# Optimization experiments

Measured on AMD Instinct MI355X. Metric: run time of the kernel, lower is better.

The kernel has to match this reference:

```python
import jax, jax.numpy as jnp
import numpy as np

T, B, D = 256, 64, 512


def setup_inputs() -> dict:
    key = jax.random.key(0)
    ks = jax.random.split(key, 9)
    s = 1.0 / np.sqrt(D)  # torch Linear default init scale (uniform), use scaled normal
    return {
        "x": jax.random.normal(ks[0], (T, B, D), dtype=jnp.float32),
        "y": jax.random.normal(ks[1], (T, B, D), dtype=jnp.float32),
        "Wr": jax.random.normal(ks[2], (D, D), dtype=jnp.float32) * s,
        "Ur": jax.random.normal(ks[3], (D, D), dtype=jnp.float32) * s,
        "Wz": jax.random.normal(ks[4], (D, D), dtype=jnp.float32) * s,
        "Uz": jax.random.normal(ks[5], (D, D), dtype=jnp.float32) * s,
        "Wg": jax.random.normal(ks[6], (D, D), dtype=jnp.float32) * s,
        "Ug": jax.random.normal(ks[7], (D, D), dtype=jnp.float32) * s,
        "bg": jnp.full((D,), 2.0, dtype=jnp.float32),
    }


def reference(x, y, Wr, Ur, Wz, Uz, Wg, Ug, bg):
    # GTrXL gating unit. torch Linear(y) == y @ W.T
    r = jax.nn.sigmoid(jnp.einsum("tbd,ed->tbe", y, Wr) + jnp.einsum("tbd,ed->tbe", x, Ur))
    z = jax.nn.sigmoid(jnp.einsum("tbd,ed->tbe", y, Wz) + jnp.einsum("tbd,ed->tbe", x, Uz) - bg)
    h = jnp.tanh(jnp.einsum("tbd,ed->tbe", y, Wg) + jnp.einsum("tbd,ed->tbe", r * x, Ug))
    g = (1.0 - z) * x + z * h  # (T, B, D)
    return g
```

## Files before the change

### kernel.cpp

```cpp
#include <hip/hip_runtime.h>
#include <stdint.h>

typedef unsigned short u16;
typedef __attribute__((ext_vector_type(8))) __bf16 bf16x8;
typedef __attribute__((ext_vector_type(4))) float f32x4;

#define Tn 256
#define Bn 64
#define Dn 512
#define Mn (Tn * Bn)


__device__ __forceinline__ u16 f2bf(float f) {
  unsigned u = __float_as_uint(f);
  u += 0x7fffu + ((u >> 16) & 1u);
  return (u16)(u >> 16);
}

__device__ __forceinline__ void async16(const u16* g, u16* l) {
  __builtin_amdgcn_global_load_lds(
      (const __attribute__((address_space(1))) unsigned int*)g,
      (__attribute__((address_space(3))) unsigned int*)l, 16, 0, 0);
}

__device__ __forceinline__ float sigmoidf_(float v) {
  return 1.f / (1.f + __expf(-v));
}


__global__ void cast_xy(const float* __restrict__ y, const float* __restrict__ x,
                        u16* __restrict__ yb, u16* __restrict__ xb) {
  int b = blockIdx.x;
  const float* src;
  u16* dst;
  if (b < 8192) { src = y; dst = yb; }
  else          { src = x; dst = xb; b -= 8192; }
  const int i4 = b * 256 + (int)threadIdx.x;
  float4 v = ((const float4*)src)[i4];
  ushort4 o;
  o.x = f2bf(v.x); o.y = f2bf(v.y); o.z = f2bf(v.z); o.w = f2bf(v.w);
  ((ushort4*)dst)[i4] = o;
}

__global__ void cast_w6(const float* w0, const float* w1, const float* w2,
                        const float* w3, const float* w4, const float* w5,
                        u16* __restrict__ wb) {
  const int b = blockIdx.x;
  const int wi = b >> 8, bb = b & 255;
  const float* src = wi == 0 ? w0 : wi == 1 ? w1 : wi == 2 ? w2
                   : wi == 3 ? w3 : wi == 4 ? w4 : w5;
  const int i4 = bb * 256 + (int)threadIdx.x;
  float4 v = ((const float4*)src)[i4];
  ushort4 o;
  o.x = f2bf(v.x); o.y = f2bf(v.y); o.z = f2bf(v.z); o.w = f2bf(v.w);
  ((ushort4*)(wb + wi * 262144))[i4] = o;
}

__global__ __launch_bounds__(256, 2) void gemm_rz(
    const u16* __restrict__ yb, const u16* __restrict__ xb,
    const u16* __restrict__ wb,
    const float* __restrict__ xf, const float* __restrict__ bg,
    u16* __restrict__ rxb, float* __restrict__ zf) {
  __shared__ u16 sY[128 * 64];
  __shared__ u16 sX[128 * 64];
  __shared__ u16 sW[4 * 64 * 64];

  const int tid = threadIdx.x;
  const int lane = tid & 63;
  const int wave = tid >> 6;
  const int waveM = wave >> 1, waveN = wave & 1;
  const int nb = blockIdx.x & 7, mb = blockIdx.x >> 3;
  const int rowStart = mb * 128, colStart = nb * 64;
  const int rbase = tid >> 3;
  const int cbase = (tid & 7) * 8;
  const int wbyte = (tid & 192) * 16;
  const int lm = lane & 15, quad = lane >> 4;

  f32x4 accR[4][2] = {};
  f32x4 accZ[4][2] = {};

  for (int k0 = 0; k0 < Dn; k0 += 64) {
#pragma unroll
    for (int s = 0; s < 4; ++s) {
      async16(yb + (size_t)(rowStart + s * 32 + rbase) * Dn + k0 + cbase,
              (u16*)((char*)sY + s * 4096 + wbyte));
      async16(xb + (size_t)(rowStart + s * 32 + rbase) * Dn + k0 + cbase,
              (u16*)((char*)sX + s * 4096 + wbyte));
    }
#pragma unroll
    for (int w = 0; w < 4; ++w)
#pragma unroll
      for (int s = 0; s < 2; ++s)
        async16(wb + (size_t)w * 262144 +
                    (size_t)(colStart + s * 32 + rbase) * Dn + k0 + cbase,
                (u16*)((char*)sW + w * 8192 + s * 4096 + wbyte));
    __syncthreads();

#pragma unroll
    for (int kk = 0; kk < 2; ++kk) {
      bf16x8 ay[4], ax[4], bw[4][2];
#pragma unroll
      for (int i = 0; i < 4; ++i) {
        const int off = (waveM * 64 + i * 16 + lm) * 64 + kk * 32 + quad * 8;
        ay[i] = *(const bf16x8*)(sY + off);
        ax[i] = *(const bf16x8*)(sX + off);
      }
#pragma unroll
      for (int w = 0; w < 4; ++w)
#pragma unroll
        for (int j = 0; j < 2; ++j)
          bw[w][j] = *(const bf16x8*)(sW + w * 4096 +
                                      (waveN * 32 + j * 16 + lm) * 64 + kk * 32 + quad * 8);
#pragma unroll
      for (int i = 0; i < 4; ++i)
#pragma unroll
        for (int j = 0; j < 2; ++j) {
          accR[i][j] = __builtin_amdgcn_mfma_f32_16x16x32_bf16(ay[i], bw[0][j], accR[i][j], 0, 0, 0);
          accR[i][j] = __builtin_amdgcn_mfma_f32_16x16x32_bf16(ax[i], bw[1][j], accR[i][j], 0, 0, 0);
          accZ[i][j] = __builtin_amdgcn_mfma_f32_16x16x32_bf16(ay[i], bw[2][j], accZ[i][j], 0, 0, 0);
          accZ[i][j] = __builtin_amdgcn_mfma_f32_16x16x32_bf16(ax[i], bw[3][j], accZ[i][j], 0, 0, 0);
        }
    }
    __syncthreads();
  }

#pragma unroll
  for (int j = 0; j < 2; ++j) {
    const int e = colStart + waveN * 32 + j * 16 + lm;
    const float bgv = bg[e];
#pragma unroll
    for (int i = 0; i < 4; ++i) {
      const int m0 = rowStart + waveM * 64 + i * 16 + quad * 4;
#pragma unroll
      for (int rg = 0; rg < 4; ++rg) {
        const size_t idx = (size_t)(m0 + rg) * Dn + e;
        const float r = sigmoidf_(accR[i][j][rg]);
        rxb[idx] = f2bf(r * xf[idx]);
        zf[idx] = sigmoidf_(accZ[i][j][rg] - bgv);
      }
    }
  }
}

__global__ __launch_bounds__(256, 2) void gemm_g(
    const u16* __restrict__ ab, const u16* __restrict__ wg,
    float* __restrict__ outacc) {
  __shared__ u16 sA[128 * 64];
  __shared__ u16 sW[64 * 64];

  const int tid = threadIdx.x;
  const int lane = tid & 63;
  const int wave = tid >> 6;
  const int waveM = wave >> 1, waveN = wave & 1;
  const int nb = blockIdx.x & 7, mb = blockIdx.x >> 3;
  const int rowStart = mb * 128, colStart = nb * 64;
  const int rbase = tid >> 3;
  const int cbase = (tid & 7) * 8;
  const int wbyte = (tid & 192) * 16;
  const int lm = lane & 15, quad = lane >> 4;

  f32x4 acc[4][2] = {};

  for (int k0 = 0; k0 < Dn; k0 += 64) {
#pragma unroll
    for (int s = 0; s < 4; ++s)
      async16(ab + (size_t)(rowStart + s * 32 + rbase) * Dn + k0 + cbase,
              (u16*)((char*)sA + s * 4096 + wbyte));
#pragma unroll
    for (int s = 0; s < 2; ++s)
      async16(wg + (size_t)(colStart + s * 32 + rbase) * Dn + k0 + cbase,
              (u16*)((char*)sW + s * 4096 + wbyte));
    __syncthreads();

#pragma unroll
    for (int kk = 0; kk < 2; ++kk) {
      bf16x8 aa[4], bw[2];
#pragma unroll
      for (int i = 0; i < 4; ++i)
        aa[i] = *(const bf16x8*)(sA + (waveM * 64 + i * 16 + lm) * 64 + kk * 32 + quad * 8);
#pragma unroll
      for (int j = 0; j < 2; ++j)
        bw[j] = *(const bf16x8*)(sW + (waveN * 32 + j * 16 + lm) * 64 + kk * 32 + quad * 8);
#pragma unroll
      for (int i = 0; i < 4; ++i)
#pragma unroll
        for (int j = 0; j < 2; ++j)
          acc[i][j] = __builtin_amdgcn_mfma_f32_16x16x32_bf16(aa[i], bw[j], acc[i][j], 0, 0, 0);
    }
    __syncthreads();
  }

#pragma unroll
  for (int j = 0; j < 2; ++j) {
    const int e = colStart + waveN * 32 + j * 16 + lm;
#pragma unroll
    for (int i = 0; i < 4; ++i) {
      const int m0 = rowStart + waveM * 64 + i * 16 + quad * 4;
#pragma unroll
      for (int rg = 0; rg < 4; ++rg)
        outacc[(size_t)(m0 + rg) * Dn + e] = acc[i][j][rg];
    }
  }
}

__global__ __launch_bounds__(256, 2) void gemm_final(
    const u16* __restrict__ rxb, const u16* __restrict__ ug,
    const float* __restrict__ zf, const float* __restrict__ xf,
    float* __restrict__ out ) {
  __shared__ u16 sA[128 * 64];
  __shared__ u16 sW[64 * 64];

  const int tid = threadIdx.x;
  const int lane = tid & 63;
  const int wave = tid >> 6;
  const int waveM = wave >> 1, waveN = wave & 1;
  const int nb = blockIdx.x & 7, mb = blockIdx.x >> 3;
  const int rowStart = mb * 128, colStart = nb * 64;
  const int rbase = tid >> 3;
  const int cbase = (tid & 7) * 8;
  const int wbyte = (tid & 192) * 16;
  const int lm = lane & 15, quad = lane >> 4;

  f32x4 acc[4][2] = {};

  for (int k0 = 0; k0 < Dn; k0 += 64) {
#pragma unroll
    for (int s = 0; s < 4; ++s)
      async16(rxb + (size_t)(rowStart + s * 32 + rbase) * Dn + k0 + cbase,
              (u16*)((char*)sA + s * 4096 + wbyte));
#pragma unroll
    for (int s = 0; s < 2; ++s)
      async16(ug + (size_t)(colStart + s * 32 + rbase) * Dn + k0 + cbase,
              (u16*)((char*)sW + s * 4096 + wbyte));
    __syncthreads();

#pragma unroll
    for (int kk = 0; kk < 2; ++kk) {
      bf16x8 aa[4], bw[2];
#pragma unroll
      for (int i = 0; i < 4; ++i)
        aa[i] = *(const bf16x8*)(sA + (waveM * 64 + i * 16 + lm) * 64 + kk * 32 + quad * 8);
#pragma unroll
      for (int j = 0; j < 2; ++j)
        bw[j] = *(const bf16x8*)(sW + (waveN * 32 + j * 16 + lm) * 64 + kk * 32 + quad * 8);
#pragma unroll
      for (int i = 0; i < 4; ++i)
#pragma unroll
        for (int j = 0; j < 2; ++j)
          acc[i][j] = __builtin_amdgcn_mfma_f32_16x16x32_bf16(aa[i], bw[j], acc[i][j], 0, 0, 0);
    }
    __syncthreads();
  }

#pragma unroll
  for (int j = 0; j < 2; ++j) {
    const int e = colStart + waveN * 32 + j * 16 + lm;
#pragma unroll
    for (int i = 0; i < 4; ++i) {
      const int m0 = rowStart + waveM * 64 + i * 16 + quad * 4;
#pragma unroll
      for (int rg = 0; rg < 4; ++rg) {
        const size_t idx = (size_t)(m0 + rg) * Dn + e;
        const float pre = out[idx] + acc[i][j][rg];
        const float ex = __expf(-2.f * pre);
        const float h = (1.f - ex) / (1.f + ex);
        const float z = zf[idx];
        const float xv = xf[idx];
        out[idx] = (1.f - z) * xv + z * h;
      }
    }
  }
}

extern "C" void kernel_launch(void* const* d_in, const int* in_sizes, int n_in,
                              void* d_out, int out_size, void* d_ws, size_t ws_size,
                              hipStream_t stream) {
  const float* x  = (const float*)d_in[0];
  const float* y  = (const float*)d_in[1];
  const float* Wr = (const float*)d_in[2];
  const float* Ur = (const float*)d_in[3];
  const float* Wz = (const float*)d_in[4];
  const float* Uz = (const float*)d_in[5];
  const float* Wg = (const float*)d_in[6];
  const float* Ug = (const float*)d_in[7];
  const float* bg = (const float*)d_in[8];
  float* out = (float*)d_out;

  char* ws = (char*)d_ws;
  u16* yb  = (u16*)(ws);
  u16* xb  = (u16*)(ws + 16777216);
  u16* rxb = (u16*)(ws + 2 * 16777216);
  u16* wb  = (u16*)(ws + 3 * 16777216);
  float* zf = (float*)(ws + 3 * 16777216 + 3145728);

  cast_xy<<<16384, 256, 0, stream>>>(y, x, yb, xb);
  cast_w6<<<1536, 256, 0, stream>>>(Wr, Ur, Wz, Uz, Wg, Ug, wb);
  gemm_rz<<<1024, 256, 0, stream>>>(yb, xb, wb, x, bg, rxb, zf);
  gemm_g<<<1024, 256, 0, stream>>>(yb, wb + (size_t)4 * 262144, out);
  gemm_final<<<1024, 256, 0, stream>>>(rxb, wb + (size_t)5 * 262144, zf, x, out);
}
```

Before: 248.3 us.

## Fuse Wg GEMM into r/z GEMM, merge cast kernels, store z as bf16

Folds the y·Wg GEMM into the r/z kernel so the y tile already in shared memory is reused, adding a fifth weight tile and a third accumulator set. The gate pre-activation goes straight to the output buffer, and the separate gemm_g kernel and its second read of y are removed. The two cast kernels become a single launch, and z is stored as bf16 instead of fp32 to halve that traffic. In exchange the fused kernel needs more shared memory and registers, which may lower occupancy under launch_bounds(256,2), and z loses some precision.

```diff
diff --git a/kernel.cpp b/kernel.cpp
--- a/kernel.cpp
+++ b/kernel.cpp
@@ -17,6 +17,10 @@
   return (u16)(u >> 16);
 }
 
+__device__ __forceinline__ float bf2f(u16 b) {
+  return __uint_as_float(((unsigned)b) << 16);
+}
+
 __device__ __forceinline__ void async16(const u16* g, u16* l) {
   __builtin_amdgcn_global_load_lds(
       (const __attribute__((address_space(1))) unsigned int*)g,
@@ -27,14 +31,25 @@
   return 1.f / (1.f + __expf(-v));
 }
 
-
-__global__ void cast_xy(const float* __restrict__ y, const float* __restrict__ x,
-                        u16* __restrict__ yb, u16* __restrict__ xb) {
+__global__ void cast_all(const float* __restrict__ y, const float* __restrict__ x,
+                         const float* w0, const float* w1, const float* w2,
+                         const float* w3, const float* w4, const float* w5,
+                         u16* __restrict__ yb, u16* __restrict__ xb,
+                         u16* __restrict__ wb) {
   int b = blockIdx.x;
   const float* src;
   u16* dst;
-  if (b < 8192) { src = y; dst = yb; }
-  else          { src = x; dst = xb; b -= 8192; }
+  if (b < 8192) {
+    src = y; dst = yb;
+  } else if (b < 16384) {
+    src = x; dst = xb; b -= 8192;
+  } else {
+    b -= 16384;
+    const int wi = b >> 8;
+    b &= 255;
+    src = wi == 0 ? w0 : wi == 1 ? w1 : wi == 2 ? w2 : wi == 3 ? w3 : wi == 4 ? w4 : w5;
+    dst = wb + wi * 262144;
+  }
   const int i4 = b * 256 + (int)threadIdx.x;
   float4 v = ((const float4*)src)[i4];
   ushort4 o;
@@ -42,28 +57,14 @@
   ((ushort4*)dst)[i4] = o;
 }
 
-__global__ void cast_w6(const float* w0, const float* w1, const float* w2,
-                        const float* w3, const float* w4, const float* w5,
-                        u16* __restrict__ wb) {
-  const int b = blockIdx.x;
-  const int wi = b >> 8, bb = b & 255;
-  const float* src = wi == 0 ? w0 : wi == 1 ? w1 : wi == 2 ? w2
-                   : wi == 3 ? w3 : wi == 4 ? w4 : w5;
-  const int i4 = bb * 256 + (int)threadIdx.x;
-  float4 v = ((const float4*)src)[i4];
-  ushort4 o;
-  o.x = f2bf(v.x); o.y = f2bf(v.y); o.z = f2bf(v.z); o.w = f2bf(v.w);
-  ((ushort4*)(wb + wi * 262144))[i4] = o;
-}
-
-__global__ __launch_bounds__(256, 2) void gemm_rz(
+__global__ __launch_bounds__(256, 2) void gemm_rzg(
     const u16* __restrict__ yb, const u16* __restrict__ xb,
     const u16* __restrict__ wb,
     const float* __restrict__ xf, const float* __restrict__ bg,
-    u16* __restrict__ rxb, float* __restrict__ zf) {
+    u16* __restrict__ rxb, u16* __restrict__ zb, float* __restrict__ gacc) {
   __shared__ u16 sY[128 * 64];
   __shared__ u16 sX[128 * 64];
-  __shared__ u16 sW[4 * 64 * 64];
+  __shared__ u16 sW[5 * 64 * 64];
 
   const int tid = threadIdx.x;
   const int lane = tid & 63;
@@ -78,6 +79,7 @@
 
   f32x4 accR[4][2] = {};
   f32x4 accZ[4][2] = {};
+  f32x4 accG[4][2] = {};
 
   for (int k0 = 0; k0 < Dn; k0 += 64) {
 #pragma unroll
@@ -88,7 +90,7 @@
               (u16*)((char*)sX + s * 4096 + wbyte));
     }
 #pragma unroll
-    for (int w = 0; w < 4; ++w)
+    for (int w = 0; w < 5; ++w)
 #pragma unroll
       for (int s = 0; s < 2; ++s)
         async16(wb + (size_t)w * 262144 +
@@ -98,7 +100,7 @@
 
 #pragma unroll
     for (int kk = 0; kk < 2; ++kk) {
-      bf16x8 ay[4], ax[4], bw[4][2];
+      bf16x8 ay[4], ax[4], bw[5][2];
 #pragma unroll
       for (int i = 0; i < 4; ++i) {
         const int off = (waveM * 64 + i * 16 + lm) * 64 + kk * 32 + quad * 8;
@@ -106,7 +108,7 @@
         ax[i] = *(const bf16x8*)(sX + off);
       }
 #pragma unroll
-      for (int w = 0; w < 4; ++w)
+      for (int w = 0; w < 5; ++w)
 #pragma unroll
         for (int j = 0; j < 2; ++j)
           bw[w][j] = *(const bf16x8*)(sW + w * 4096 +
@@ -119,6 +121,7 @@
           accR[i][j] = __builtin_amdgcn_mfma_f32_16x16x32_bf16(ax[i], bw[1][j], accR[i][j], 0, 0, 0);
           accZ[i][j] = __builtin_amdgcn_mfma_f32_16x16x32_bf16(ay[i], bw[2][j], accZ[i][j], 0, 0, 0);
           accZ[i][j] = __builtin_amdgcn_mfma_f32_16x16x32_bf16(ax[i], bw[3][j], accZ[i][j], 0, 0, 0);
+          accG[i][j] = __builtin_amdgcn_mfma_f32_16x16x32_bf16(ay[i], bw[4][j], accG[i][j], 0, 0, 0);
         }
     }
     __syncthreads();
@@ -136,15 +139,17 @@
         const size_t idx = (size_t)(m0 + rg) * Dn + e;
         const float r = sigmoidf_(accR[i][j][rg]);
         rxb[idx] = f2bf(r * xf[idx]);
-        zf[idx] = sigmoidf_(accZ[i][j][rg] - bgv);
+        zb[idx] = f2bf(sigmoidf_(accZ[i][j][rg] - bgv));
+        gacc[idx] = accG[i][j][rg];
       }
     }
   }
 }
 
-__global__ __launch_bounds__(256, 2) void gemm_g(
-    const u16* __restrict__ ab, const u16* __restrict__ wg,
-    float* __restrict__ outacc) {
+__global__ __launch_bounds__(256, 2) void gemm_final(
+    const u16* __restrict__ rxb, const u16* __restrict__ ug,
+    const u16* __restrict__ zb, const float* __restrict__ xf,
+    float* __restrict__ out ) {
   __shared__ u16 sA[128 * 64];
   __shared__ u16 sW[64 * 64];
 
@@ -164,68 +169,6 @@
   for (int k0 = 0; k0 < Dn; k0 += 64) {
 #pragma unroll
     for (int s = 0; s < 4; ++s)
-      async16(ab + (size_t)(rowStart + s * 32 + rbase) * Dn + k0 + cbase,
-              (u16*)((char*)sA + s * 4096 + wbyte));
-#pragma unroll
-    for (int s = 0; s < 2; ++s)
-      async16(wg + (size_t)(colStart + s * 32 + rbase) * Dn + k0 + cbase,
-              (u16*)((char*)sW + s * 4096 + wbyte));
-    __syncthreads();
-
-#pragma unroll
-    for (int kk = 0; kk < 2; ++kk) {
-      bf16x8 aa[4], bw[2];
-#pragma unroll
-      for (int i = 0; i < 4; ++i)
-        aa[i] = *(const bf16x8*)(sA + (waveM * 64 + i * 16 + lm) * 64 + kk * 32 + quad * 8);
-#pragma unroll
-      for (int j = 0; j < 2; ++j)
-        bw[j] = *(const bf16x8*)(sW + (waveN * 32 + j * 16 + lm) * 64 + kk * 32 + quad * 8);
-#pragma unroll
-      for (int i = 0; i < 4; ++i)
-#pragma unroll
-        for (int j = 0; j < 2; ++j)
-          acc[i][j] = __builtin_amdgcn_mfma_f32_16x16x32_bf16(aa[i], bw[j], acc[i][j], 0, 0, 0);
-    }
-    __syncthreads();
-  }
-
-#pragma unroll
-  for (int j = 0; j < 2; ++j) {
-    const int e = colStart + waveN * 32 + j * 16 + lm;
-#pragma unroll
-    for (int i = 0; i < 4; ++i) {
-      const int m0 = rowStart + waveM * 64 + i * 16 + quad * 4;
-#pragma unroll
-      for (int rg = 0; rg < 4; ++rg)
-        outacc[(size_t)(m0 + rg) * Dn + e] = acc[i][j][rg];
-    }
-  }
-}
-
-__global__ __launch_bounds__(256, 2) void gemm_final(
-    const u16* __restrict__ rxb, const u16* __restrict__ ug,
-    const float* __restrict__ zf, const float* __restrict__ xf,
-    float* __restrict__ out ) {
-  __shared__ u16 sA[128 * 64];
-  __shared__ u16 sW[64 * 64];
-
-  const int tid = threadIdx.x;
-  const int lane = tid & 63;
-  const int wave = tid >> 6;
-  const int waveM = wave >> 1, waveN = wave & 1;
-  const int nb = blockIdx.x & 7, mb = blockIdx.x >> 3;
-  const int rowStart = mb * 128, colStart = nb * 64;
-  const int rbase = tid >> 3;
-  const int cbase = (tid & 7) * 8;
-  const int wbyte = (tid & 192) * 16;
-  const int lm = lane & 15, quad = lane >> 4;
-
-  f32x4 acc[4][2] = {};
-
-  for (int k0 = 0; k0 < Dn; k0 += 64) {
-#pragma unroll
-    for (int s = 0; s < 4; ++s)
       async16(rxb + (size_t)(rowStart + s * 32 + rbase) * Dn + k0 + cbase,
               (u16*)((char*)sA + s * 4096 + wbyte));
 #pragma unroll
@@ -264,7 +207,7 @@
         const float pre = out[idx] + acc[i][j][rg];
         const float ex = __expf(-2.f * pre);
         const float h = (1.f - ex) / (1.f + ex);
-        const float z = zf[idx];
+        const float z = bf2f(zb[idx]);
         const float xv = xf[idx];
         out[idx] = (1.f - z) * xv + z * h;
       }
@@ -291,11 +234,9 @@
   u16* xb  = (u16*)(ws + 16777216);
   u16* rxb = (u16*)(ws + 2 * 16777216);
   u16* wb  = (u16*)(ws + 3 * 16777216);
-  float* zf = (float*)(ws + 3 * 16777216 + 3145728);
-
-  cast_xy<<<16384, 256, 0, stream>>>(y, x, yb, xb);
-  cast_w6<<<1536, 256, 0, stream>>>(Wr, Ur, Wz, Uz, Wg, Ug, wb);
-  gemm_rz<<<1024, 256, 0, stream>>>(yb, xb, wb, x, bg, rxb, zf);
-  gemm_g<<<1024, 256, 0, stream>>>(yb, wb + (size_t)4 * 262144, out);
-  gemm_final<<<1024, 256, 0, stream>>>(rxb, wb + (size_t)5 * 262144, zf, x, out);
-}
+  u16* zb  = (u16*)(ws + 3 * 16777216 + 3145728);
+
+  cast_all<<<17920, 256, 0, stream>>>(y, x, Wr, Ur, Wz, Uz, Wg, Ug, yb, xb, wb);
+  gemm_rzg<<<1024, 256, 0, stream>>>(yb, xb, wb, x, bg, rxb, zb, out);
+  gemm_final<<<1024, 256, 0, stream>>>(rxb, wb + (size_t)5 * 262144, zb, x, out);
+}
```

Measured after the change: 228.7 us. 7.9% less time.
